# Kernel optimization log

Measured on AMD Instinct MI355X. Metric: run time of the kernel, lower is better.

The kernel has to match this reference:

```python
import math
import jax, jax.numpy as jnp
import numpy as np

VOCAB = 30522
HIDDEN = 768
TYPE_VOCAB = 2
EPS = 1e-12
MAX_LEN = 5000


def sin_table(dim, max_len=MAX_LEN):
    pos = jnp.arange(max_len, dtype=jnp.float32)[:, None]
    div = jnp.exp(jnp.arange(0, dim, 2, dtype=jnp.float32) * (-(math.log(10000.0) / dim)))
    ang = pos * div  # [max_len, dim//2]
    pe = jnp.zeros((max_len, dim), dtype=jnp.float32)
    pe = pe.at[:, 0::2].set(jnp.sin(ang))
    pe = pe.at[:, 1::2].set(jnp.cos(ang))
    return pe


def setup_inputs() -> dict:
    key = jax.random.key(0)
    k1, k2, k3, k4, k5, k6, k7 = jax.random.split(key, 7)
    B, S = 8, 4096
    input_ids = jax.random.randint(k1, (B, S), 0, VOCAB, dtype=jnp.int64 if jax.config.jax_enable_x64 else jnp.int32)
    tok_struct_vec = jax.random.randint(k2, (B, S, 3), 0, S, dtype=input_ids.dtype)
    sent_struct_vec = jax.random.randint(k3, (B, 64, 2), 0, 64, dtype=input_ids.dtype)
    token_type_ids = jax.random.randint(k4, (B, S), 0, TYPE_VOCAB, dtype=input_ids.dtype)
    word_emb = jax.random.normal(k5, (VOCAB, HIDDEN), dtype=jnp.float32) * 0.02
    word_emb = word_emb.at[0].set(0.0)  # padding_idx=0
    type_emb = jax.random.normal(k6, (TYPE_VOCAB, HIDDEN), dtype=jnp.float32) * 0.02
    ln_w = jnp.ones((HIDDEN,), dtype=jnp.float32)
    ln_b = jnp.zeros((HIDDEN,), dtype=jnp.float32)
    return {"input_ids": input_ids, "tok_struct_vec": tok_struct_vec,
            "sent_struct_vec": sent_struct_vec, "token_type_ids": token_type_ids,
            "word_emb": word_emb, "type_emb": type_emb, "ln_w": ln_w, "ln_b": ln_b}


def reference(input_ids, tok_struct_vec, sent_struct_vec, token_type_ids,
              word_emb, type_emb, ln_w, ln_b):
    B, S = input_ids.shape
    pe = sin_table(HIDDEN)[:S]            # [S, H]
    hs_pe = sin_table(HIDDEN // 3)[:S]    # [S, H/3]

    words = word_emb[input_ids]           # [B,S,H]
    tt = type_emb[token_type_ids]         # [B,S,H]

    # NOTE: faithful to source bug: compute_se closes over para_pos, so all
    # three struct embeddings gather with para_pos (tok_struct_vec[:,:,0]).
    para_pos = tok_struct_vec[:, :, 0]
    g = hs_pe[para_pos]                   # [B,S,H/3]
    struct = jnp.concatenate((g, g, g), axis=2)  # [B,S,H]

    emb = words + pe[None, :, :] + tt + struct
    mu = jnp.mean(emb, axis=-1, keepdims=True)
    var = jnp.mean(jnp.square(emb - mu), axis=-1, keepdims=True)
    out = (emb - mu) / jnp.sqrt(var + EPS) * ln_w + ln_b
    return out  # dropout is identity in eval mode
```

## Files before the change

### kernel.cpp

```cpp
#include <hip/hip_runtime.h>
#include <math.h>

#define HIDDEN 768

#define NEG_LN1E4_OVER_768 (-0.011992630692677323f)
#define NEG_LN1E4_OVER_256 (-0.035977892078031970f)

__global__ __launch_bounds__(256) void emb_ln_kernel(
    const int*   __restrict__ input_ids,
    const int*   __restrict__ tok_struct,
    const int*   __restrict__ token_type,
    const float* __restrict__ word_emb,
    const float* __restrict__ type_emb,
    const float* __restrict__ ln_w,
    const float* __restrict__ ln_b,
    float*       __restrict__ out,
    int S)
{
    const int row = blockIdx.x;
    const int s   = row & (S - 1);
    const int t   = threadIdx.x;

    const int id   = input_ids[row];
    const int tt   = token_type[row];
    const int ppos = tok_struct[row * 3];

    const float div_hs = __expf((float)(t & ~1) * NEG_LN1E4_OVER_256);
    const float ang_hs = (float)ppos * div_hs;
    const float hsv = (t & 1) ? __cosf(ang_hs) : __sinf(ang_hs);

    const size_t wbase = (size_t)id * HIDDEN;
    const size_t tbase = (size_t)tt * HIDDEN;

    float v[3];
#pragma unroll
    for (int j = 0; j < 3; ++j) {
        const int h = t + j * 256;
        const float div_pe = __expf((float)(h & ~1) * NEG_LN1E4_OVER_768);
        const float ang_pe = (float)s * div_pe;
        const float pev = (h & 1) ? __cosf(ang_pe) : __sinf(ang_pe);
        v[j] = word_emb[wbase + h] + type_emb[tbase + h] + pev + hsv;
    }

    float s1 = v[0] + v[1] + v[2];
    float s2 = v[0] * v[0] + v[1] * v[1] + v[2] * v[2];

#pragma unroll
    for (int off = 32; off > 0; off >>= 1) {
        s1 += __shfl_down(s1, off, 64);
        s2 += __shfl_down(s2, off, 64);
    }

    __shared__ float ls1[4], ls2[4];
    const int wave = t >> 6;
    const int lane = t & 63;
    if (lane == 0) { ls1[wave] = s1; ls2[wave] = s2; }
    __syncthreads();

    const float fs1 = ls1[0] + ls1[1] + ls1[2] + ls1[3];
    const float fs2 = ls2[0] + ls2[1] + ls2[2] + ls2[3];

    const float inv_n = 1.0f / (float)HIDDEN;
    const float mu  = fs1 * inv_n;
    float var = fs2 * inv_n - mu * mu;
    var = fmaxf(var, 0.0f);
    const float rstd = rsqrtf(var + 1e-12f);

    const size_t obase = (size_t)row * HIDDEN;
#pragma unroll
    for (int j = 0; j < 3; ++j) {
        const int h = t + j * 256;
        out[obase + h] = (v[j] - mu) * rstd * ln_w[h] + ln_b[h];
    }
}

extern "C" void kernel_launch(void* const* d_in, const int* in_sizes, int n_in,
                              void* d_out, int out_size, void* d_ws, size_t ws_size,
                              hipStream_t stream) {
    const int*   input_ids  = (const int*)  d_in[0];
    const int*   tok_struct = (const int*)  d_in[1];
    const int*   token_type = (const int*)  d_in[3];
    const float* word_emb   = (const float*)d_in[4];
    const float* type_emb   = (const float*)d_in[5];
    const float* ln_w       = (const float*)d_in[6];
    const float* ln_b       = (const float*)d_in[7];
    float* out = (float*)d_out;

    const int BS = in_sizes[0];
    const int B  = in_sizes[2] / 128;
    const int S  = BS / B;

    emb_ln_kernel<<<BS, 256, 0, stream>>>(input_ids, tok_struct, token_type,
                                          word_emb, type_emb, ln_w, ln_b,
                                          out, S);
}
```

Before: 198.1 us.

## Map one wavefront per row with float4 loads and shuffle-only reduction

Each 256-thread block now handles four rows, one per wavefront, and each lane owns four contiguous floats per chunk, read and written as float4. The LayerNorm reduction stays entirely inside the wave through xor shuffles, which removes the shared-memory exchange and the __syncthreads barrier. Positional-encoding exponentials are computed once per lane and rescaled by constant factors for the other chunks, cutting transcendental work. The scaled-exponent shortcut changes rounding slightly, and the launch assumes BS is divisible by 4.

Result: faster. 191.4 us (-3.4%).

```diff
diff --git a/kernel.cpp b/kernel.cpp
--- a/kernel.cpp
+++ b/kernel.cpp
@@ -3,8 +3,10 @@
 
 #define HIDDEN 768
 
-#define NEG_LN1E4_OVER_768 (-0.011992630692677323f)
-#define NEG_LN1E4_OVER_256 (-0.035977892078031970f)
+#define K768 (-0.011992630692677323f)
+#define K256 (-0.035977892078031970f)
+#define C256 (0.04641588833612779f)
+#define C512 (0.002154434690031884f)
 
 __global__ __launch_bounds__(256) void emb_ln_kernel(
     const int*   __restrict__ input_ids,
@@ -17,60 +19,84 @@
     float*       __restrict__ out,
     int S)
 {
-    const int row = blockIdx.x;
-    const int s   = row & (S - 1);
-    const int t   = threadIdx.x;
+    const int wave = threadIdx.x >> 6;
+    const int lane = threadIdx.x & 63;
+    const int row  = blockIdx.x * 4 + wave;
+    const int s    = row & (S - 1);
 
     const int id   = input_ids[row];
     const int tt   = token_type[row];
     const int ppos = tok_struct[row * 3];
 
-    const float div_hs = __expf((float)(t & ~1) * NEG_LN1E4_OVER_256);
-    const float ang_hs = (float)ppos * div_hs;
-    const float hsv = (t & 1) ? __cosf(ang_hs) : __sinf(ang_hs);
+    const int h0 = lane * 4;
 
-    const size_t wbase = (size_t)id * HIDDEN;
-    const size_t tbase = (size_t)tt * HIDDEN;
+    const float d0 = __expf((float)h0 * K256);
+    const float d1 = __expf((float)(h0 + 2) * K256);
+    const float pp = (float)ppos;
+    float hs[4];
+    hs[0] = __sinf(pp * d0);
+    hs[1] = __cosf(pp * d0);
+    hs[2] = __sinf(pp * d1);
+    hs[3] = __cosf(pp * d1);
 
-    float v[3];
+    const float e0 = __expf((float)h0 * K768);
+    const float e2 = __expf((float)(h0 + 2) * K768);
+    const float fs = (float)s;
+
+    const float4* wrow = (const float4*)(word_emb + (size_t)id * HIDDEN);
+    const float4* trow = (const float4*)(type_emb + (size_t)tt * HIDDEN);
+
+    float v[12];
 #pragma unroll
     for (int j = 0; j < 3; ++j) {
-        const int h = t + j * 256;
-        const float div_pe = __expf((float)(h & ~1) * NEG_LN1E4_OVER_768);
-        const float ang_pe = (float)s * div_pe;
-        const float pev = (h & 1) ? __cosf(ang_pe) : __sinf(ang_pe);
-        v[j] = word_emb[wbase + h] + type_emb[tbase + h] + pev + hsv;
+        const float scale = (j == 0) ? 1.0f : (j == 1 ? C256 : C512);
+        const float a0 = fs * (e0 * scale);
+        const float a1 = fs * (e2 * scale);
+        const float pe0 = __sinf(a0);
+        const float pe1 = __cosf(a0);
+        const float pe2 = __sinf(a1);
+        const float pe3 = __cosf(a1);
+
+        const float4 w  = wrow[lane + 64 * j];
+        const float4 ty = trow[lane + 64 * j];
+
+        v[4 * j + 0] = w.x + ty.x + pe0 + hs[0];
+        v[4 * j + 1] = w.y + ty.y + pe1 + hs[1];
+        v[4 * j + 2] = w.z + ty.z + pe2 + hs[2];
+        v[4 * j + 3] = w.w + ty.w + pe3 + hs[3];
     }
 
-    float s1 = v[0] + v[1] + v[2];
-    float s2 = v[0] * v[0] + v[1] * v[1] + v[2] * v[2];
-
+    float s1 = 0.0f, s2 = 0.0f;
 #pragma unroll
-    for (int off = 32; off > 0; off >>= 1) {
-        s1 += __shfl_down(s1, off, 64);
-        s2 += __shfl_down(s2, off, 64);
+    for (int i = 0; i < 12; ++i) {
+        s1 += v[i];
+        s2 = fmaf(v[i], v[i], s2);
+    }
+#pragma unroll
+    for (int off = 1; off < 64; off <<= 1) {
+        s1 += __shfl_xor(s1, off, 64);
+        s2 += __shfl_xor(s2, off, 64);
     }
 
-    __shared__ float ls1[4], ls2[4];
-    const int wave = t >> 6;
-    const int lane = t & 63;
-    if (lane == 0) { ls1[wave] = s1; ls2[wave] = s2; }
-    __syncthreads();
-
-    const float fs1 = ls1[0] + ls1[1] + ls1[2] + ls1[3];
-    const float fs2 = ls2[0] + ls2[1] + ls2[2] + ls2[3];
-
     const float inv_n = 1.0f / (float)HIDDEN;
-    const float mu  = fs1 * inv_n;
-    float var = fs2 * inv_n - mu * mu;
+    const float mu  = s1 * inv_n;
+    float var = s2 * inv_n - mu * mu;
     var = fmaxf(var, 0.0f);
     const float rstd = rsqrtf(var + 1e-12f);
 
-    const size_t obase = (size_t)row * HIDDEN;
+    const float4* wv = (const float4*)ln_w;
+    const float4* bv = (const float4*)ln_b;
+    float4* orow = (float4*)(out + (size_t)row * HIDDEN);
 #pragma unroll
     for (int j = 0; j < 3; ++j) {
-        const int h = t + j * 256;
-        out[obase + h] = (v[j] - mu) * rstd * ln_w[h] + ln_b[h];
+        const float4 g = wv[lane + 64 * j];
+        const float4 b = bv[lane + 64 * j];
+        float4 r;
+        r.x = (v[4 * j + 0] - mu) * rstd * g.x + b.x;
+        r.y = (v[4 * j + 1] - mu) * rstd * g.y + b.y;
+        r.z = (v[4 * j + 2] - mu) * rstd * g.z + b.z;
+        r.w = (v[4 * j + 3] - mu) * rstd * g.w + b.w;
+        orow[lane + 64 * j] = r;
     }
 }
 
@@ -90,7 +116,7 @@
     const int B  = in_sizes[2] / 128;
     const int S  = BS / B;
 
-    emb_ln_kernel<<<BS, 256, 0, stream>>>(input_ids, tok_struct, token_type,
-                                          word_emb, type_emb, ln_w, ln_b,
-                                          out, S);
+    emb_ln_kernel<<<BS / 4, 256, 0, stream>>>(input_ids, tok_struct, token_type,
+                                              word_emb, type_emb, ln_w, ln_b,
+                                              out, S);
 }
```
